# Optimization experiments

Hardware: AMD Instinct MI355X
Metric: run time of the kernel (lower is better)

The kernel has to match this reference:

```python
import jax, jax.numpy as jnp
import numpy as np

S = 2048          # total tokens (prefill, batch 1)
HID = 2560        # hidden_size
H = 32            # num query heads
HK = 8            # num kv heads
HD = 128          # head_dim
Q_SIZE = H * HD   # 4096
KV_SIZE = HK * HD # 1024
EPS = 1e-6
THETA = 10000.0
SCALE = HD ** -0.5


def setup_inputs() -> dict:
    key = jax.random.key(0)
    k1, k2, k3 = jax.random.split(key, 3)
    return {
        "positions": jnp.arange(S, dtype=jnp.int64 if jax.config.jax_enable_x64 else jnp.int32),
        "hidden_states": jax.random.normal(k1, (S, HID), dtype=jnp.float32),
        "w_qkv": jax.random.normal(k2, (Q_SIZE + 2 * KV_SIZE, HID), dtype=jnp.float32) * 0.02,
        "w_o": jax.random.normal(k3, (HID, Q_SIZE), dtype=jnp.float32) * 0.02,
        "q_norm_w": jnp.ones((HD,), dtype=jnp.float32),
        "k_norm_w": jnp.ones((HD,), dtype=jnp.float32),
    }


def _rmsnorm(x, w):
    # x: [..., HD]; computed in fp32 as torch RMSNorm does
    var = jnp.mean(jnp.square(x.astype(jnp.float32)), axis=-1, keepdims=True)
    return (x * jax.lax.rsqrt(var + EPS) * w).astype(x.dtype)


def _rope(x, cos, sin):
    # NEOX-style rotate-half, x: [S, nH, HD], cos/sin: [S, 1, HD//2]
    x1, x2 = x[..., : HD // 2], x[..., HD // 2:]
    return jnp.concatenate([x1 * cos - x2 * sin, x2 * cos + x1 * sin], axis=-1)


def reference(positions, hidden_states, w_qkv, w_o, q_norm_w, k_norm_w):
    # QKV projection (no bias)
    qkv = hidden_states @ w_qkv.T                               # [S, Q+2KV]
    q, k, v = jnp.split(qkv, [Q_SIZE, Q_SIZE + KV_SIZE], axis=-1)
    q = _rmsnorm(q.reshape(S, H, HD), q_norm_w)                 # per-head q RMSNorm
    k = _rmsnorm(k.reshape(S, HK, HD), k_norm_w)                # per-head k RMSNorm
    v = v.reshape(S, HK, HD)

    # RoPE
    inv_freq = 1.0 / (THETA ** (jnp.arange(0, HD, 2, dtype=jnp.float32) / HD))  # [HD/2]
    ang = positions.astype(jnp.float32)[:, None] * inv_freq     # [S, HD/2]
    cos, sin = jnp.cos(ang)[:, None, :], jnp.sin(ang)[:, None, :]
    q = _rope(q, cos, sin)
    k = _rope(k, cos, sin)

    # GQA: expand kv heads to query heads (group size G = H // HK)
    G = H // HK
    qg = q.reshape(S, HK, G, HD)
    scores = jnp.einsum("qhgd,khd->hgqk", qg, k) * SCALE        # [HK, G, S, S]
    causal = jnp.tril(jnp.ones((S, S), dtype=bool))
    scores = jnp.where(causal, scores, jnp.float32(-1e30))
    probs = jax.nn.softmax(scores, axis=-1)
    o = jnp.einsum("hgqk,khd->qhgd", probs, v).reshape(S, Q_SIZE)
    return o @ w_o.T                                            # [S, HID]
```

## Files before the change

### kernel.cpp

```cpp
#include <hip/hip_runtime.h>
#include <hip/hip_bf16.h>

typedef __bf16 bf16x8 __attribute__((ext_vector_type(8)));
typedef __bf16 bf16x4 __attribute__((ext_vector_type(4)));
typedef float f32x4 __attribute__((ext_vector_type(4)));

#define S_LEN 2048
#define HID 2560
#define NH 32
#define NKV 8
#define HD 128
#define QSZ 4096
#define KVSZ 1024
#define QKV_N 6144
#define SCALE_Q 0.08838834764831845f
#define LOG2_THETA 13.287712379549449f

__global__ void castk(const float* __restrict__ in, __bf16* __restrict__ out, int n4) {
  int i = blockIdx.x * blockDim.x + threadIdx.x;
  int stride = gridDim.x * blockDim.x;
  for (; i < n4; i += stride) {
    float4 v = ((const float4*)in)[i];
    bf16x4 o;
    o[0] = (__bf16)v.x; o[1] = (__bf16)v.y; o[2] = (__bf16)v.z; o[3] = (__bf16)v.w;
    ((bf16x4*)out)[i] = o;
  }
}

__device__ __forceinline__ void gload16(const void* g, void* l) {
  __builtin_amdgcn_global_load_lds((const __attribute__((address_space(1))) void*)g,
                                   (__attribute__((address_space(3))) void*)l, 16, 0, 0);
}

__global__ __launch_bounds__(256, 2) void gemm_bt(
    const __bf16* __restrict__ A, const __bf16* __restrict__ B, float* __restrict__ C,
    int M, int N, int K) {
  __shared__ __attribute__((aligned(16))) __bf16 lta[128 * 32];
  __shared__ __attribute__((aligned(16))) __bf16 ltb[128 * 32];
  const int t = threadIdx.x, w = t >> 6, l = t & 63;
  const int bn = blockIdx.x, bm = blockIdx.y;
  const int wr = w >> 1, wc = w & 1;
  const int lg = l >> 4, li = l & 15;

  f32x4 acc[4][4];
#pragma unroll
  for (int i = 0; i < 4; ++i)
#pragma unroll
    for (int j = 0; j < 4; ++j) acc[i][j] = (f32x4){0.f, 0.f, 0.f, 0.f};

  const int nkt = K >> 5;
  const int c0 = w * 2, c1 = w * 2 + 1;
  const int row0 = c0 * 16 + (l >> 2), row1 = c1 * 16 + (l >> 2);
  const int cole = (l & 3) * 8;
  const __bf16* ga = A + (size_t)(bm * 128) * K + cole;
  const __bf16* gb = B + (size_t)(bn * 128) * K + cole;

  for (int kt = 0; kt < nkt; ++kt) {
    const size_t ko = (size_t)kt * 32;
    gload16(ga + (size_t)row0 * K + ko, &lta[c0 * 512]);
    gload16(gb + (size_t)row0 * K + ko, &ltb[c0 * 512]);
    gload16(ga + (size_t)row1 * K + ko, &lta[c1 * 512]);
    gload16(gb + (size_t)row1 * K + ko, &ltb[c1 * 512]);
    __syncthreads();
    bf16x8 af[4], bfr[4];
#pragma unroll
    for (int f = 0; f < 4; ++f) {
      af[f]  = *(const bf16x8*)&lta[(wr * 64 + f * 16 + li) * 32 + lg * 8];
      bfr[f] = *(const bf16x8*)&ltb[(wc * 64 + f * 16 + li) * 32 + lg * 8];
    }
#pragma unroll
    for (int fm = 0; fm < 4; ++fm)
#pragma unroll
      for (int fn = 0; fn < 4; ++fn)
        acc[fm][fn] = __builtin_amdgcn_mfma_f32_16x16x32_bf16(af[fm], bfr[fn], acc[fm][fn], 0, 0, 0);
    __syncthreads();
  }

  float* cp = C + (size_t)(bm * 128 + wr * 64 + lg * 4) * N + bn * 128 + wc * 64 + li;
#pragma unroll
  for (int fm = 0; fm < 4; ++fm)
#pragma unroll
    for (int fn = 0; fn < 4; ++fn)
#pragma unroll
      for (int r = 0; r < 4; ++r)
        cp[(size_t)(fm * 16 + r) * N + fn * 16] = acc[fm][fn][r];
}

__global__ __launch_bounds__(64) void norm_rope(
    const float* __restrict__ qkv, const int* __restrict__ positions,
    const float* __restrict__ qw, const float* __restrict__ kw,
    __bf16* __restrict__ q_bf, __bf16* __restrict__ k_bf) {
  const int s = blockIdx.x, hh = blockIdx.y, l = threadIdx.x;
  const float* row;
  const float* wgt;
  __bf16* outp;
  float scale;
  if (hh < NH) {
    row = qkv + (size_t)s * QKV_N + hh * HD;
    wgt = qw;
    outp = q_bf + ((size_t)s * NH + hh) * HD;
    scale = SCALE_Q;
  } else {
    row = qkv + (size_t)s * QKV_N + QSZ + (hh - NH) * HD;
    wgt = kw;
    outp = k_bf + ((size_t)s * NKV + (hh - NH)) * HD;
    scale = 1.0f;
  }
  float x1 = row[l], x2 = row[l + 64];
  float ss = x1 * x1 + x2 * x2;
#pragma unroll
  for (int off = 32; off; off >>= 1) ss += __shfl_xor(ss, off, 64);
  float rs = rsqrtf(ss * (1.0f / 128.0f) + 1e-6f);
  float n1 = x1 * rs * wgt[l], n2 = x2 * rs * wgt[l + 64];
  float ang = (float)positions[s] * exp2f((float)l * (-LOG2_THETA / 64.0f));
  float sn, cs;
  sincosf(ang, &sn, &cs);
  outp[l]      = (__bf16)((n1 * cs - n2 * sn) * scale);
  outp[l + 64] = (__bf16)((n2 * cs + n1 * sn) * scale);
}

__global__ __launch_bounds__(256) void v_prep(const float* __restrict__ qkv, __bf16* __restrict__ vt) {
  const int s0 = blockIdx.x * 32, hk = blockIdx.y;
  __shared__ float lv[32][129];
  const int t = threadIdx.x;
  {
    const int s = t >> 3, dseg = (t & 7) * 16;
    const float* src = qkv + (size_t)(s0 + s) * QKV_N + (QSZ + KVSZ) + hk * HD + dseg;
#pragma unroll
    for (int j = 0; j < 4; ++j) {
      float4 v = *(const float4*)(src + j * 4);
      lv[s][dseg + j * 4 + 0] = v.x;
      lv[s][dseg + j * 4 + 1] = v.y;
      lv[s][dseg + j * 4 + 2] = v.z;
      lv[s][dseg + j * 4 + 3] = v.w;
    }
  }
  __syncthreads();
  {
    const int d = t >> 1, sh = (t & 1) * 16;
    bf16x8 a, b;
#pragma unroll
    for (int j = 0; j < 8; ++j) {
      a[j] = (__bf16)lv[sh + j][d];
      b[j] = (__bf16)lv[sh + 8 + j][d];
    }
    __bf16* dst = vt + ((size_t)hk * HD + d) * S_LEN + s0 + sh;
    *(bf16x8*)dst = a;
    *(bf16x8*)(dst + 8) = b;
  }
}

__global__ __launch_bounds__(256, 3) void flash_attn(
    const __bf16* __restrict__ q_bf, const __bf16* __restrict__ k_bf,
    const __bf16* __restrict__ vt_bf, __bf16* __restrict__ o_bf) {
  const int t = threadIdx.x;
  const int w = t >> 6, l = t & 63;
  const int b = blockIdx.x;
  const int hk = b & 7;
  const int rem = b >> 3;
  const int h = hk * 4 + (rem & 3);
  const int qtile = 31 - (rem >> 2);
  const int q0 = qtile * 64 + w * 16;
  const int lg = l >> 4, li = l & 15;

  __shared__ __attribute__((aligned(16))) __bf16 k_lds[2][32 * 128];
  __shared__ __attribute__((aligned(16))) __bf16 v_lds[2][128 * 32];
  __shared__ __attribute__((aligned(16))) __bf16 p_lds[4][16][40];

  bf16x8 bq[4];
  {
    const __bf16* qp = q_bf + ((size_t)(q0 + li) * NH + h) * HD + lg * 8;
#pragma unroll
    for (int c = 0; c < 4; ++c) bq[c] = *(const bf16x8*)(qp + c * 32);
  }

  float m_r = -1e30f, l_r = 0.f;
  f32x4 o_acc[8];
#pragma unroll
  for (int fd = 0; fd < 8; ++fd) o_acc[fd] = (f32x4){0.f, 0.f, 0.f, 0.f};

  const int nkt = 2 * qtile + 2;

  auto STAGE = [&](int buf, int kb) {
#pragma unroll
    for (int j = 0; j < 2; ++j) {
      const int key = (t >> 4) + j * 16;
      const int csrc = (t & 15) ^ (key & 7);
      gload16(k_bf + (size_t)(kb * 32 + key) * KVSZ + hk * HD + csrc * 8,
              &k_lds[buf][j * 2048 + w * 512]);
    }
#pragma unroll
    for (int j = 0; j < 2; ++j) {
      const int d = (t >> 2) + j * 64;
      const int csrc = (t & 3) ^ (d & 3);
      gload16(vt_bf + ((size_t)hk * HD + d) * S_LEN + kb * 32 + csrc * 8,
              &v_lds[buf][j * 2048 + w * 512]);
    }
  };

  STAGE(0, 0);
  for (int kb = 0; kb < nkt; ++kb) {
    __syncthreads();
    if (kb + 1 < nkt) STAGE((kb + 1) & 1, kb + 1);
    const int cur = kb & 1;

    bf16x8 kr[8];
#pragma unroll
    for (int c = 0; c < 4; ++c) {
      const int ch = ((c * 4 + lg) ^ (li & 7)) * 8;
      kr[c]     = *(const bf16x8*)&k_lds[cur][li * 128 + ch];
      kr[c + 4] = *(const bf16x8*)&k_lds[cur][(li + 16) * 128 + ch];
    }
    f32x4 s0 = {0.f, 0.f, 0.f, 0.f}, s1 = {0.f, 0.f, 0.f, 0.f};
#pragma unroll
    for (int c = 0; c < 4; ++c) {
      s0 = __builtin_amdgcn_mfma_f32_16x16x32_bf16(kr[c],     bq[c], s0, 0, 0, 0);
      s1 = __builtin_amdgcn_mfma_f32_16x16x32_bf16(kr[c + 4], bq[c], s1, 0, 0, 0);
    }
    const int q = q0 + li;
    const int key0 = kb * 32 + lg * 4;
    float v0[4], v1[4];
#pragma unroll
    for (int r = 0; r < 4; ++r) {
      v0[r] = (key0 + r      <= q) ? s0[r] : -1e30f;
      v1[r] = (key0 + r + 16 <= q) ? s1[r] : -1e30f;
    }
    float tm = fmaxf(fmaxf(fmaxf(v0[0], v0[1]), fmaxf(v0[2], v0[3])),
                     fmaxf(fmaxf(v1[0], v1[1]), fmaxf(v1[2], v1[3])));
    tm = fmaxf(tm, __shfl_xor(tm, 16));
    tm = fmaxf(tm, __shfl_xor(tm, 32));
    float mn = fmaxf(m_r, tm);
    float sc = __expf(m_r - mn);
    float e0[4], e1[4], ps = 0.f;
#pragma unroll
    for (int r = 0; r < 4; ++r) {
      e0[r] = __expf(v0[r] - mn);
      e1[r] = __expf(v1[r] - mn);
      ps += e0[r] + e1[r];
    }
    ps += __shfl_xor(ps, 16);
    ps += __shfl_xor(ps, 32);
    l_r = l_r * sc + ps;
    m_r = mn;
#pragma unroll
    for (int r = 0; r < 4; ++r) {
      float scq = __shfl(sc, lg * 4 + r, 16);
#pragma unroll
      for (int fd = 0; fd < 8; ++fd) o_acc[fd][r] *= scq;
    }
    bf16x4 pw0, pw1;
#pragma unroll
    for (int r = 0; r < 4; ++r) { pw0[r] = (__bf16)e0[r]; pw1[r] = (__bf16)e1[r]; }
    *(bf16x4*)&p_lds[w][li][lg * 4]      = pw0;
    *(bf16x4*)&p_lds[w][li][lg * 4 + 16] = pw1;
    bf16x8 pa = *(const bf16x8*)&p_lds[w][li][lg * 8];
#pragma unroll
    for (int fd = 0; fd < 8; ++fd) {
      bf16x8 bv = *(const bf16x8*)&v_lds[cur][(fd * 16 + li) * 32 + ((lg ^ (li & 3)) * 8)];
      o_acc[fd] = __builtin_amdgcn_mfma_f32_16x16x32_bf16(pa, bv, o_acc[fd], 0, 0, 0);
    }
  }

  const size_t obase = (size_t)(q0 + lg * 4) * QSZ + (size_t)h * HD + li;
#pragma unroll
  for (int r = 0; r < 4; ++r) {
    float inv = 1.0f / __shfl(l_r, lg * 4 + r, 16);
#pragma unroll
    for (int fd = 0; fd < 8; ++fd)
      o_bf[obase + (size_t)r * QSZ + fd * 16] = (__bf16)(o_acc[fd][r] * inv);
  }
}

extern "C" void kernel_launch(void* const* d_in, const int* in_sizes, int n_in,
                              void* d_out, int out_size, void* d_ws, size_t ws_size,
                              hipStream_t stream) {
  const int*   positions = (const int*)d_in[0];
  const float* hidden    = (const float*)d_in[1];
  const float* w_qkv     = (const float*)d_in[2];
  const float* w_o       = (const float*)d_in[3];
  const float* q_norm_w  = (const float*)d_in[4];
  const float* k_norm_w  = (const float*)d_in[5];
  float* out = (float*)d_out;

  char* p = (char*)d_ws;
  float*  qkv = (float*)p;   p += (size_t)S_LEN * QKV_N * 4;
  __bf16* hs  = (__bf16*)p;  p += (size_t)S_LEN * HID * 2;
  __bf16* wq  = (__bf16*)p;  p += (size_t)QKV_N * HID * 2;
  __bf16* wo  = (__bf16*)p;  p += (size_t)HID * QSZ * 2;
  __bf16* qb  = (__bf16*)p;  p += (size_t)S_LEN * QSZ * 2;
  __bf16* kb  = (__bf16*)p;  p += (size_t)S_LEN * KVSZ * 2;
  __bf16* vt  = (__bf16*)p;  p += (size_t)NKV * HD * S_LEN * 2;
  __bf16* ob  = (__bf16*)p;  p += (size_t)S_LEN * QSZ * 2;

  castk<<<2048, 256, 0, stream>>>(hidden, hs, S_LEN * HID / 4);
  castk<<<2048, 256, 0, stream>>>(w_qkv, wq, QKV_N * HID / 4);
  castk<<<2048, 256, 0, stream>>>(w_o, wo, HID * QSZ / 4);

  gemm_bt<<<dim3(QKV_N / 128, S_LEN / 128), 256, 0, stream>>>(hs, wq, qkv, S_LEN, QKV_N, HID);

  norm_rope<<<dim3(S_LEN, NH + NKV), 64, 0, stream>>>(qkv, positions, q_norm_w, k_norm_w, qb, kb);
  v_prep<<<dim3(S_LEN / 32, NKV), 256, 0, stream>>>(qkv, vt);

  flash_attn<<<1024, 256, 0, stream>>>(qb, kb, vt, ob);

  gemm_bt<<<dim3(HID / 128, S_LEN / 128), 256, 0, stream>>>(ob, wo, out, S_LEN, HID, QSZ);
}
```

Measured before the change: 432.6 us.

## Replace QKV projection GEMM with 256x256-tile, 512-thread pipelined kernel

Adds a new bf16 GEMM kernel with 256x256 output tiles, 8 waves and 128 KB of dynamic LDS. It uses a double-buffered K pipeline that issues async global-to-LDS loads six stages ahead, with explicit vmcnt waits, barriers and setprio around the MFMA blocks. The QKV projection now uses this kernel, aiming for more operand reuse per LDS load and better overlap of memory and compute. The output projection still uses the old kernel. The large LDS footprint and only 24x8 = 192 blocks raise occupancy and tail-wave risks, and the hand-placed waitcnt logic must stay correct for K=2560.

```diff
diff --git a/kernel.cpp b/kernel.cpp
--- a/kernel.cpp
+++ b/kernel.cpp
@@ -16,6 +16,9 @@
 #define SCALE_Q 0.08838834764831845f
 #define LOG2_THETA 13.287712379549449f
 
+#define ASM_VMCNT(n) asm volatile("s_waitcnt vmcnt(" #n ")" ::: "memory")
+#define ASM_BAR()    asm volatile("s_barrier" ::: "memory")
+
 __global__ void castk(const float* __restrict__ in, __bf16* __restrict__ out, int n4) {
   int i = blockIdx.x * blockDim.x + threadIdx.x;
   int stride = gridDim.x * blockDim.x;
@@ -30,6 +33,88 @@
 __device__ __forceinline__ void gload16(const void* g, void* l) {
   __builtin_amdgcn_global_load_lds((const __attribute__((address_space(1))) void*)g,
                                    (__attribute__((address_space(3))) void*)l, 16, 0, 0);
+}
+
+__global__ __launch_bounds__(512, 2) void gemm256(
+    const __bf16* __restrict__ A, const __bf16* __restrict__ B, float* __restrict__ C,
+    int M, int N, int K) {
+  extern __shared__ __bf16 lds[];
+  const int t = threadIdx.x, w = t >> 6, l = t & 63;
+  const int wr = w >> 2, wc = w & 3;
+  const int lg = l >> 4, li = l & 15;
+  const int bn = blockIdx.x, bm = blockIdx.y;
+  const int NKT = K >> 6;
+
+  f32x4 acc[8][4];
+#pragma unroll
+  for (int i = 0; i < 8; ++i)
+#pragma unroll
+    for (int j = 0; j < 4; ++j) acc[i][j] = (f32x4){0.f, 0.f, 0.f, 0.f};
+
+  auto STG = [&](int n) {
+    const int kt = n >> 2, h = n & 3;
+    const int kcol = kt * 64 + (h >> 1) * 32;
+    __bf16* dst = &lds[(size_t)(((kt & 1) << 2) + h) << 13];
+    const __bf16* srcb = (h & 1) ? (B + (size_t)(bn * 256) * K)
+                                 : (A + (size_t)(bm * 256) * K);
+#pragma unroll
+    for (int j = 0; j < 2; ++j) {
+      const int idx = j * 512 + t;
+      const int row = idx >> 2;
+      const int col = (((idx & 3) ^ (row & 3)) << 3);
+      gload16(srcb + (size_t)row * K + kcol + col,
+              dst + j * 4096 + w * 512);
+    }
+  };
+  auto RD = [&](int buf, int h, int lrow) -> bf16x8 {
+    const int off = (lrow << 5) + ((lg ^ (lrow & 3)) << 3);
+    return *(const bf16x8*)&lds[((size_t)(((buf << 2) + h)) << 13) + off];
+  };
+
+  for (int n = 0; n < 6; ++n) STG(n);
+  ASM_VMCNT(8);
+  ASM_BAR();
+
+  for (int kt = 0; kt < NKT; ++kt) {
+    const int buf = kt & 1;
+#pragma unroll
+    for (int q = 0; q < 4; ++q) {
+      const int ks = q >> 1, mh = q & 1;
+      bf16x8 a[4], b[4];
+#pragma unroll
+      for (int i = 0; i < 4; ++i)
+        a[i] = RD(buf, ks * 2,     wr * 128 + mh * 64 + i * 16 + li);
+#pragma unroll
+      for (int j = 0; j < 4; ++j)
+        b[j] = RD(buf, ks * 2 + 1, wc * 64 + j * 16 + li);
+      const int s = kt * 4 + q;
+      if (s + 6 < NKT * 4) STG(s + 6);
+      ASM_BAR();
+      __builtin_amdgcn_s_setprio(1);
+#pragma unroll
+      for (int i = 0; i < 4; ++i)
+#pragma unroll
+        for (int j = 0; j < 4; ++j)
+          acc[mh * 4 + i][j] = __builtin_amdgcn_mfma_f32_16x16x32_bf16(
+              a[i], b[j], acc[mh * 4 + i][j], 0, 0, 0);
+      __builtin_amdgcn_s_setprio(0);
+      if (q & 1) {
+        if (s < 4 * NKT - 5)       ASM_VMCNT(8);
+        else if (s == 4 * NKT - 5) ASM_VMCNT(4);
+        else if (s == 4 * NKT - 3) ASM_VMCNT(0);
+      }
+      ASM_BAR();
+    }
+  }
+
+  float* cp = C + (size_t)(bm * 256 + wr * 128 + lg * 4) * N + bn * 256 + wc * 64 + li;
+#pragma unroll
+  for (int fm = 0; fm < 8; ++fm)
+#pragma unroll
+    for (int fn = 0; fn < 4; ++fn)
+#pragma unroll
+      for (int r = 0; r < 4; ++r)
+        cp[(size_t)(fm * 16 + r) * N + fn * 16] = acc[fm][fn][r];
 }
 
 __global__ __launch_bounds__(256, 2) void gemm_bt(
@@ -296,7 +381,10 @@
   castk<<<2048, 256, 0, stream>>>(w_qkv, wq, QKV_N * HID / 4);
   castk<<<2048, 256, 0, stream>>>(w_o, wo, HID * QSZ / 4);
 
-  gemm_bt<<<dim3(QKV_N / 128, S_LEN / 128), 256, 0, stream>>>(hs, wq, qkv, S_LEN, QKV_N, HID);
+  hipFuncSetAttribute((const void*)gemm256,
+                      hipFuncAttributeMaxDynamicSharedMemorySize, 131072);
+  gemm256<<<dim3(QKV_N / 256, S_LEN / 256), 512, 131072, stream>>>(
+      hs, wq, qkv, S_LEN, QKV_N, HID);
 
   norm_rope<<<dim3(S_LEN, NH + NKV), 64, 0, stream>>>(qkv, positions, q_norm_w, k_norm_w, qb, kb);
   v_prep<<<dim3(S_LEN / 32, NKV), 256, 0, stream>>>(qkv, vt);
```

New measurement: 448.8 us. +3.7%, slower.
